# Kernel optimization log

Measured on AMD Instinct MI355X. Metric: run time of the kernel, lower is better.

Reference implementation:

```python
import jax, jax.numpy as jnp
import numpy as np

N = 6144
INPUT_SIZE = 1024
HIDDEN = 256
NEG_INF = -9e15  # matches torch masked_fill value -9000000000000000.0


def setup_inputs() -> dict:
    key = jax.random.key(0)
    k1, k2, k3, k4 = jax.random.split(key, 4)
    nodes_embed = jax.random.normal(k1, (N, INPUT_SIZE), dtype=jnp.float32)
    node_adj = jax.random.randint(k2, (N, N), 0, 2, dtype=jnp.int32)
    # learned params (xavier-uniform-ish scaling)
    limW = np.sqrt(6.0 / (INPUT_SIZE + HIDDEN))
    W = jax.random.uniform(k3, (INPUT_SIZE, HIDDEN), minval=-limW, maxval=limW, dtype=jnp.float32)
    lima = 1.414 * np.sqrt(6.0 / (2 * HIDDEN + 1))
    a_edge = jax.random.uniform(k4, (2 * HIDDEN,), minval=-lima, maxval=lima, dtype=jnp.float32)
    return {"nodes_embed": nodes_embed, "W": W, "a_edge": a_edge, "node_adj": node_adj}


def reference(nodes_embed, W, a_edge, node_adj):
    # h = nodes_embed @ W : [N, hidden]
    h = nodes_embed @ W
    # W_edge([h_i ; h_j]) decomposes exactly: (h_i @ a1) + (h_j @ a2)
    a1, a2 = a_edge[:HIDDEN], a_edge[HIDDEN:]
    score = (h @ a1)[:, None] + (h @ a2)[None, :]  # [N, N]
    adj_f = node_adj.astype(h.dtype)
    weight = jax.nn.leaky_relu(adj_f * score, negative_slope=0.2)
    weight = jnp.where(node_adj == 0, jnp.asarray(NEG_INF, h.dtype), weight)
    attention = jax.nn.softmax(weight, axis=-1)
    # dropout in eval mode (identity)
    return attention @ h  # [N, hidden]
```

## Files before the change

### kernel.cpp

```cpp
#include <hip/hip_runtime.h>
#include <hip/hip_bf16.h>

#define NN 6144
#define INPUT 1024
#define HID 256

using frag  = __attribute__((ext_vector_type(8))) short;
using f32x4 = __attribute__((ext_vector_type(4))) float;

static __device__ __forceinline__ unsigned short bf16u(float x) {
    unsigned u = __float_as_uint(x);
    u += 0x7fff + ((u >> 16) & 1);
    return (unsigned short)(u >> 16);
}

static __device__ __forceinline__ void gll16(const void* g, void* l) {
    __builtin_amdgcn_global_load_lds((__attribute__((address_space(1))) const void*)g,
                                     (__attribute__((address_space(3))) void*)l, 16, 0, 0);
}
static __device__ __forceinline__ void gll4(const void* g, void* l) {
    __builtin_amdgcn_global_load_lds((__attribute__((address_space(1))) const void*)g,
                                     (__attribute__((address_space(3))) void*)l, 4, 0, 0);
}

static __device__ __forceinline__ void lds_barrier() {
    asm volatile("s_waitcnt lgkmcnt(0)" ::: "memory");
    __builtin_amdgcn_s_barrier();
    __builtin_amdgcn_sched_barrier(0);
}

__global__ __launch_bounds__(256) void k_prep(const float* __restrict__ X,
                                              const float* __restrict__ W,
                                              unsigned short* __restrict__ Xb,
                                              unsigned short* __restrict__ Wt) {
    int b = blockIdx.x;
    if (b < 3072) {
        int t = b * 256 + threadIdx.x;
        const float4* p = reinterpret_cast<const float4*>(X) + (size_t)t * 2;
        float4 x0 = p[0], x1 = p[1];
        frag v;
        v[0] = (short)bf16u(x0.x); v[1] = (short)bf16u(x0.y);
        v[2] = (short)bf16u(x0.z); v[3] = (short)bf16u(x0.w);
        v[4] = (short)bf16u(x1.x); v[5] = (short)bf16u(x1.y);
        v[6] = (short)bf16u(x1.z); v[7] = (short)bf16u(x1.w);
        *reinterpret_cast<frag*>(Xb + (size_t)t * 8) = v;
    } else {
        int t = (b - 3072) * 256 + threadIdx.x;
        int n = t >> 10, k = t & 1023;
        Wt[t] = bf16u(W[k * HID + n]);
    }
}

__global__ __launch_bounds__(256, 4) void k_gemm1(const unsigned short* __restrict__ Xb,
                                                  const unsigned short* __restrict__ Wt,
                                                  const float* __restrict__ a_edge,
                                                  unsigned short* __restrict__ hT,
                                                  float* __restrict__ s1,
                                                  float* __restrict__ s2) {
    __shared__ unsigned short A[2][32][128];
    int t = threadIdx.x;
    int i0 = blockIdx.x * 32, n0 = blockIdx.y * 64;
    int w = t >> 6, l = t & 63, lm = l & 15, q = l >> 4;
    int nw = n0 + w * 16;

    const unsigned short* brow = Wt + (size_t)(nw + lm) * INPUT + q * 8;

    int r0 = w * 8 + (l >> 4);
    const unsigned short* xs0 = Xb + (size_t)(i0 + r0) * INPUT + (((l & 15) ^ (r0 & 7)) << 3);
    const unsigned short* xs1 = Xb + (size_t)(i0 + r0 + 4) * INPUT + (((l & 15) ^ ((r0 + 4) & 7)) << 3);

#define GSTAGE(C, BUF) { \
        gll16(xs0 + (C) * 128, &A[BUF][w * 8][0]); \
        gll16(xs1 + (C) * 128, &A[BUF][w * 8 + 4][0]); }

    f32x4 acc0 = {}, acc1 = {};
    GSTAGE(0, 0)

    for (int c = 0; c < 8; c++) {
        int buf = c & 1;
        frag b0 = *reinterpret_cast<const frag*>(brow + c * 128);
        frag b1 = *reinterpret_cast<const frag*>(brow + c * 128 + 32);
        frag b2 = *reinterpret_cast<const frag*>(brow + c * 128 + 64);
        frag b3 = *reinterpret_cast<const frag*>(brow + c * 128 + 96);
        asm volatile("s_waitcnt vmcnt(4)" ::: "memory");
        __builtin_amdgcn_s_barrier();
        __builtin_amdgcn_sched_barrier(0);
        if (c < 7) GSTAGE(c + 1, buf ^ 1)

#pragma unroll
        for (int kk = 0; kk < 4; kk++) {
            int sw = (kk * 32 + q * 8) ^ ((lm & 7) << 3);
            frag a0 = *reinterpret_cast<const frag*>(&A[buf][lm][sw]);
            frag a1 = *reinterpret_cast<const frag*>(&A[buf][16 + lm][sw]);
            frag b  = (kk == 0) ? b0 : (kk == 1) ? b1 : (kk == 2) ? b2 : b3;
            acc0 = __builtin_amdgcn_mfma_f32_16x16x32_bf16(a0, b, acc0, 0, 0, 0);
            acc1 = __builtin_amdgcn_mfma_f32_16x16x32_bf16(a1, b, acc1, 0, 0, 0);
        }
    }
#undef GSTAGE

    ushort4 o;
    o.x = bf16u(acc0[0]); o.y = bf16u(acc0[1]); o.z = bf16u(acc0[2]); o.w = bf16u(acc0[3]);
    *reinterpret_cast<ushort4*>(hT + (size_t)(nw + lm) * NN + i0 + q * 4) = o;
    o.x = bf16u(acc1[0]); o.y = bf16u(acc1[1]); o.z = bf16u(acc1[2]); o.w = bf16u(acc1[3]);
    *reinterpret_cast<ushort4*>(hT + (size_t)(nw + lm) * NN + i0 + 16 + q * 4) = o;

    float a1v = a_edge[nw + lm], a2v = a_edge[HID + nw + lm];
#pragma unroll
    for (int h = 0; h < 2; h++) {
        const f32x4& ac = h ? acc1 : acc0;
#pragma unroll
        for (int r = 0; r < 4; r++) {
            float v1 = ac[r] * a1v, v2 = ac[r] * a2v;
            v1 += __shfl_xor(v1, 1); v2 += __shfl_xor(v2, 1);
            v1 += __shfl_xor(v1, 2); v2 += __shfl_xor(v2, 2);
            v1 += __shfl_xor(v1, 4); v2 += __shfl_xor(v2, 4);
            v1 += __shfl_xor(v1, 8); v2 += __shfl_xor(v2, 8);
            if (lm == 0) {
                atomicAdd(&s1[i0 + h * 16 + q * 4 + r], v1);
                atomicAdd(&s2[i0 + h * 16 + q * 4 + r], v2);
            }
        }
    }
}

__global__ __launch_bounds__(512, 2) void k_attn(const int* __restrict__ adj,
                                                 const float* __restrict__ s1,
                                                 const float* __restrict__ s2,
                                                 const unsigned short* __restrict__ hT,
                                                 float* __restrict__ U4,
                                                 float* __restrict__ denom4) {
    __shared__ unsigned short P[2][32][136];
    __shared__ int   adjS[2][32][128];
    __shared__ float s2S[2][128];
    int t = threadIdx.x;
    int m = t >> 4, cg = t & 15;
    int i0 = blockIdx.x * 32;
    int q4 = blockIdx.y, j0 = q4 * 1536;
    int w = t >> 6, l = t & 63, lm = l & 15, q = l >> 4;

    float s1v = s1[i0 + m];
    const int*   astage = adj + (size_t)(i0 + w * 4 + (l >> 5)) * NN + j0 + (l & 31) * 4;
    const float* sstage = s2 + j0 + w * 16 + l;

    const unsigned short* brow[2];
#pragma unroll
    for (int nt = 0; nt < 2; nt++)
        brow[nt] = hT + (size_t)(w * 32 + nt * 16 + lm) * NN + j0 + q * 8;

    f32x4 acc[2][2] = {};
    float dsum = 0.f;

#define STAGE(JC, BUF) { \
        gll16(astage + (JC), &adjS[BUF][w * 4][0]); \
        gll16(astage + (JC) + 2 * NN, &adjS[BUF][w * 4 + 2][0]); \
        if (l < 16) gll4(sstage + (JC), &s2S[BUF][w * 16]); }

    STAGE(0, 0)

    for (int c = 0; c < 12; c++) {
        int buf = c & 1, jc = c * 128;

        frag bf[8];
#pragma unroll
        for (int kk = 0; kk < 4; kk++)
#pragma unroll
            for (int nt = 0; nt < 2; nt++)
                bf[kk * 2 + nt] = *reinterpret_cast<const frag*>(brow[nt] + jc + kk * 32);

        asm volatile("s_waitcnt vmcnt(8)" ::: "memory");
        __builtin_amdgcn_s_barrier();
        __builtin_amdgcn_sched_barrier(0);
        if (c < 11) STAGE(jc + 128, buf ^ 1)

        {
            const int*   aL = &adjS[buf][m][cg * 8];
            const float* sL = &s2S[buf][cg * 8];
            int4   av0 = *reinterpret_cast<const int4*>(aL);
            int4   av1 = *reinterpret_cast<const int4*>(aL + 4);
            float4 sv0 = *reinterpret_cast<const float4*>(sL);
            float4 sv1 = *reinterpret_cast<const float4*>(sL + 4);
            float sc, wv, p0, p1, p2, p3, p4, p5, p6, p7;
            sc = s1v + sv0.x; wv = fmaxf(sc, 0.2f * sc); p0 = av0.x ? __expf(wv) : 0.f;
            sc = s1v + sv0.y; wv = fmaxf(sc, 0.2f * sc); p1 = av0.y ? __expf(wv) : 0.f;
            sc = s1v + sv0.z; wv = fmaxf(sc, 0.2f * sc); p2 = av0.z ? __expf(wv) : 0.f;
            sc = s1v + sv0.w; wv = fmaxf(sc, 0.2f * sc); p3 = av0.w ? __expf(wv) : 0.f;
            sc = s1v + sv1.x; wv = fmaxf(sc, 0.2f * sc); p4 = av1.x ? __expf(wv) : 0.f;
            sc = s1v + sv1.y; wv = fmaxf(sc, 0.2f * sc); p5 = av1.y ? __expf(wv) : 0.f;
            sc = s1v + sv1.z; wv = fmaxf(sc, 0.2f * sc); p6 = av1.z ? __expf(wv) : 0.f;
            sc = s1v + sv1.w; wv = fmaxf(sc, 0.2f * sc); p7 = av1.w ? __expf(wv) : 0.f;
            dsum += ((p0 + p1) + (p2 + p3)) + ((p4 + p5) + (p6 + p7));
            frag pk;
            pk[0] = (short)bf16u(p0); pk[1] = (short)bf16u(p1);
            pk[2] = (short)bf16u(p2); pk[3] = (short)bf16u(p3);
            pk[4] = (short)bf16u(p4); pk[5] = (short)bf16u(p5);
            pk[6] = (short)bf16u(p6); pk[7] = (short)bf16u(p7);
            *reinterpret_cast<frag*>(&P[buf][m][cg * 8]) = pk;
        }

        lds_barrier();

        __builtin_amdgcn_s_setprio(1);
#pragma unroll
        for (int kk = 0; kk < 4; kk++) {
            frag a0 = *reinterpret_cast<const frag*>(&P[buf][lm][kk * 32 + q * 8]);
            frag a1 = *reinterpret_cast<const frag*>(&P[buf][16 + lm][kk * 32 + q * 8]);
#pragma unroll
            for (int nt = 0; nt < 2; nt++) {
                acc[0][nt] = __builtin_amdgcn_mfma_f32_16x16x32_bf16(a0, bf[kk * 2 + nt], acc[0][nt], 0, 0, 0);
                acc[1][nt] = __builtin_amdgcn_mfma_f32_16x16x32_bf16(a1, bf[kk * 2 + nt], acc[1][nt], 0, 0, 0);
            }
        }
        __builtin_amdgcn_s_setprio(0);
    }
#undef STAGE

    float v = dsum;
    v += __shfl_xor(v, 1); v += __shfl_xor(v, 2);
    v += __shfl_xor(v, 4); v += __shfl_xor(v, 8);
    if (cg == 0) denom4[(size_t)q4 * NN + i0 + m] = v;

    float* Ub = U4 + (size_t)q4 * NN * HID;
#pragma unroll
    for (int h = 0; h < 2; h++)
#pragma unroll
        for (int nt = 0; nt < 2; nt++)
#pragma unroll
            for (int r = 0; r < 4; r++)
                Ub[(size_t)(i0 + h * 16 + q * 4 + r) * HID + w * 32 + nt * 16 + lm] = acc[h][nt][r];
}

__global__ __launch_bounds__(256) void k_norm(const float* __restrict__ U4,
                                              const float* __restrict__ denom4,
                                              float* __restrict__ out) {
    int i = blockIdx.x, t = threadIdx.x;
    size_t S = (size_t)NN * HID;
    size_t base = (size_t)i * HID + t;
    float u = U4[base] + U4[base + S] + U4[base + 2 * S] + U4[base + 3 * S];
    float d = denom4[i] + denom4[i + NN] + denom4[i + 2 * NN] + denom4[i + 3 * NN];
    out[base] = (d != 0.f) ? u / d : 0.f;
}

extern "C" void kernel_launch(void* const* d_in, const int* in_sizes, int n_in,
                              void* d_out, int out_size, void* d_ws, size_t ws_size,
                              hipStream_t stream) {
    const float* X      = (const float*)d_in[0];
    const float* W      = (const float*)d_in[1];
    const float* a_edge = (const float*)d_in[2];
    const int*   adj    = (const int*)d_in[3];
    float* out = (float*)d_out;

    float* U4     = (float*)d_ws;
    float* denom4 = U4 + (size_t)4 * NN * HID;
    float* s1     = denom4 + (size_t)4 * NN;
    float* s2     = s1 + NN;
    unsigned short* hT = (unsigned short*)(s2 + NN);
    unsigned short* Wt = hT + (size_t)HID * NN;
    unsigned short* Xb = (unsigned short*)U4;

    hipMemsetAsync(s1, 0, 2 * NN * sizeof(float), stream);
    k_prep<<<3072 + INPUT * HID / 256, 256, 0, stream>>>(X, W, Xb, Wt);
    k_gemm1<<<dim3(NN / 32, HID / 64), 256, 0, stream>>>(Xb, Wt, a_edge, hT, s1, s2);
    k_attn<<<dim3(NN / 32, 4), 512, 0, stream>>>(adj, s1, s2, hT, U4, denom4);
    k_norm<<<NN, 256, 0, stream>>>(U4, denom4, out);
}
```

Baseline: 307.2 us.

## Pre-pack X, W and h into MFMA fragment tiles and drop LDS staging

The prep kernel now writes X and W in bf16 packed 16x32 fragment tiles, so each lane's MFMA operand sits in one contiguous 16-byte chunk. gemm1 streams these fragments straight from global memory into registers with a three-deep register prefetch, replacing the LDS double buffer and its barriers. gemm1 also writes h in the same fragment-tiled layout, and the attention kernel's B-operand loads become fully coalesced 512-element tile reads. The goal is to cut LDS traffic, barriers and strided global reads. In exchange, the W transpose in prep uses strided scalar reads, and the prefetch depth is fixed.

```diff
diff --git a/kernel.cpp b/kernel.cpp
--- a/kernel.cpp
+++ b/kernel.cpp
@@ -29,83 +29,81 @@
     __builtin_amdgcn_sched_barrier(0);
 }
 
+
 __global__ __launch_bounds__(256) void k_prep(const float* __restrict__ X,
                                               const float* __restrict__ W,
-                                              unsigned short* __restrict__ Xb,
-                                              unsigned short* __restrict__ Wt) {
+                                              unsigned short* __restrict__ Xbp,
+                                              unsigned short* __restrict__ Wtp) {
     int b = blockIdx.x;
     if (b < 3072) {
         int t = b * 256 + threadIdx.x;
-        const float4* p = reinterpret_cast<const float4*>(X) + (size_t)t * 2;
+        int i = t >> 7, k8 = t & 127;
+        const float4* p = reinterpret_cast<const float4*>(X + (size_t)i * INPUT + k8 * 8);
         float4 x0 = p[0], x1 = p[1];
         frag v;
         v[0] = (short)bf16u(x0.x); v[1] = (short)bf16u(x0.y);
         v[2] = (short)bf16u(x0.z); v[3] = (short)bf16u(x0.w);
         v[4] = (short)bf16u(x1.x); v[5] = (short)bf16u(x1.y);
         v[6] = (short)bf16u(x1.z); v[7] = (short)bf16u(x1.w);
-        *reinterpret_cast<frag*>(Xb + (size_t)t * 8) = v;
+        size_t off = ((size_t)((i >> 4) * 32 + (k8 >> 2))) * 512 + (k8 & 3) * 128 + (i & 15) * 8;
+        *reinterpret_cast<frag*>(Xbp + off) = v;
     } else {
-        int t = (b - 3072) * 256 + threadIdx.x;
-        int n = t >> 10, k = t & 1023;
-        Wt[t] = bf16u(W[k * HID + n]);
-    }
-}
-
-__global__ __launch_bounds__(256, 4) void k_gemm1(const unsigned short* __restrict__ Xb,
-                                                  const unsigned short* __restrict__ Wt,
+        int u = (b - 3072) * 256 + threadIdx.x;
+        int n = u >> 7, k8 = u & 127;
+        int k = k8 * 8;
+        frag v;
+#pragma unroll
+        for (int e = 0; e < 8; e++) v[e] = (short)bf16u(W[(size_t)(k + e) * HID + n]);
+        size_t off = ((size_t)((n >> 4) * 32 + (k8 >> 2))) * 512 + (k8 & 3) * 128 + (n & 15) * 8;
+        *reinterpret_cast<frag*>(Wtp + off) = v;
+    }
+}
+
+__global__ __launch_bounds__(256, 4) void k_gemm1(const unsigned short* __restrict__ Xbp,
+                                                  const unsigned short* __restrict__ Wtp,
                                                   const float* __restrict__ a_edge,
-                                                  unsigned short* __restrict__ hT,
+                                                  unsigned short* __restrict__ hTp,
                                                   float* __restrict__ s1,
                                                   float* __restrict__ s2) {
-    __shared__ unsigned short A[2][32][128];
     int t = threadIdx.x;
-    int i0 = blockIdx.x * 32, n0 = blockIdx.y * 64;
     int w = t >> 6, l = t & 63, lm = l & 15, q = l >> 4;
-    int nw = n0 + w * 16;
-
-    const unsigned short* brow = Wt + (size_t)(nw + lm) * INPUT + q * 8;
-
-    int r0 = w * 8 + (l >> 4);
-    const unsigned short* xs0 = Xb + (size_t)(i0 + r0) * INPUT + (((l & 15) ^ (r0 & 7)) << 3);
-    const unsigned short* xs1 = Xb + (size_t)(i0 + r0 + 4) * INPUT + (((l & 15) ^ ((r0 + 4) & 7)) << 3);
-
-#define GSTAGE(C, BUF) { \
-        gll16(xs0 + (C) * 128, &A[BUF][w * 8][0]); \
-        gll16(xs1 + (C) * 128, &A[BUF][w * 8 + 4][0]); }
+    int bx = blockIdx.x, by = blockIdx.y;
+    int i0 = bx * 32;
+    int tn = by * 4 + w;
+
+    const unsigned short* pA0 = Xbp + (size_t)(bx * 2) * 32 * 512 + l * 8;
+    const unsigned short* pA1 = Xbp + (size_t)(bx * 2 + 1) * 32 * 512 + l * 8;
+    const unsigned short* pB  = Wtp + (size_t)tn * 32 * 512 + l * 8;
 
     f32x4 acc0 = {}, acc1 = {};
-    GSTAGE(0, 0)
-
-    for (int c = 0; c < 8; c++) {
-        int buf = c & 1;
-        frag b0 = *reinterpret_cast<const frag*>(brow + c * 128);
-        frag b1 = *reinterpret_cast<const frag*>(brow + c * 128 + 32);
-        frag b2 = *reinterpret_cast<const frag*>(brow + c * 128 + 64);
-        frag b3 = *reinterpret_cast<const frag*>(brow + c * 128 + 96);
-        asm volatile("s_waitcnt vmcnt(4)" ::: "memory");
-        __builtin_amdgcn_s_barrier();
-        __builtin_amdgcn_sched_barrier(0);
-        if (c < 7) GSTAGE(c + 1, buf ^ 1)
-
-#pragma unroll
-        for (int kk = 0; kk < 4; kk++) {
-            int sw = (kk * 32 + q * 8) ^ ((lm & 7) << 3);
-            frag a0 = *reinterpret_cast<const frag*>(&A[buf][lm][sw]);
-            frag a1 = *reinterpret_cast<const frag*>(&A[buf][16 + lm][sw]);
-            frag b  = (kk == 0) ? b0 : (kk == 1) ? b1 : (kk == 2) ? b2 : b3;
-            acc0 = __builtin_amdgcn_mfma_f32_16x16x32_bf16(a0, b, acc0, 0, 0, 0);
-            acc1 = __builtin_amdgcn_mfma_f32_16x16x32_bf16(a1, b, acc1, 0, 0, 0);
-        }
-    }
-#undef GSTAGE
-
+    frag a0s[3], a1s[3], bs[3];
+#pragma unroll
+    for (int s = 0; s < 2; s++) {
+        a0s[s] = *reinterpret_cast<const frag*>(pA0 + s * 512);
+        a1s[s] = *reinterpret_cast<const frag*>(pA1 + s * 512);
+        bs[s]  = *reinterpret_cast<const frag*>(pB  + s * 512);
+    }
+#pragma unroll
+    for (int tk = 0; tk < 32; tk++) {
+        int cur = tk % 3;
+        if (tk < 30) {
+            int nx = (tk + 2) % 3;
+            a0s[nx] = *reinterpret_cast<const frag*>(pA0 + (tk + 2) * 512);
+            a1s[nx] = *reinterpret_cast<const frag*>(pA1 + (tk + 2) * 512);
+            bs[nx]  = *reinterpret_cast<const frag*>(pB  + (tk + 2) * 512);
+        }
+        acc0 = __builtin_amdgcn_mfma_f32_16x16x32_bf16(a0s[cur], bs[cur], acc0, 0, 0, 0);
+        acc1 = __builtin_amdgcn_mfma_f32_16x16x32_bf16(a1s[cur], bs[cur], acc1, 0, 0, 0);
+    }
+
+    unsigned short* tb = hTp + ((size_t)bx * 16 + tn) * 512;
     ushort4 o;
     o.x = bf16u(acc0[0]); o.y = bf16u(acc0[1]); o.z = bf16u(acc0[2]); o.w = bf16u(acc0[3]);
-    *reinterpret_cast<ushort4*>(hT + (size_t)(nw + lm) * NN + i0 + q * 4) = o;
+    *reinterpret_cast<ushort4*>(tb + (q >> 1) * 128 + lm * 8 + (q & 1) * 4) = o;
     o.x = bf16u(acc1[0]); o.y = bf16u(acc1[1]); o.z = bf16u(acc1[2]); o.w = bf16u(acc1[3]);
-    *reinterpret_cast<ushort4*>(hT + (size_t)(nw + lm) * NN + i0 + 16 + q * 4) = o;
-
-    float a1v = a_edge[nw + lm], a2v = a_edge[HID + nw + lm];
+    *reinterpret_cast<ushort4*>(tb + (2 + (q >> 1)) * 128 + lm * 8 + (q & 1) * 4) = o;
+
+    float a1v = a_edge[tn * 16 + lm], a2v = a_edge[HID + tn * 16 + lm];
 #pragma unroll
     for (int h = 0; h < 2; h++) {
         const f32x4& ac = h ? acc1 : acc0;
@@ -127,7 +125,7 @@
 __global__ __launch_bounds__(512, 2) void k_attn(const int* __restrict__ adj,
                                                  const float* __restrict__ s1,
                                                  const float* __restrict__ s2,
-                                                 const unsigned short* __restrict__ hT,
+                                                 const unsigned short* __restrict__ hTp,
                                                  float* __restrict__ U4,
                                                  float* __restrict__ denom4) {
     __shared__ unsigned short P[2][32][136];
@@ -143,10 +141,8 @@
     const int*   astage = adj + (size_t)(i0 + w * 4 + (l >> 5)) * NN + j0 + (l & 31) * 4;
     const float* sstage = s2 + j0 + w * 16 + l;
 
-    const unsigned short* brow[2];
-#pragma unroll
-    for (int nt = 0; nt < 2; nt++)
-        brow[nt] = hT + (size_t)(w * 32 + nt * 16 + lm) * NN + j0 + q * 8;
+    const unsigned short* hb = hTp + (size_t)(w * 2) * 512 + l * 8;
+    int tjb = q4 * 48;
 
     f32x4 acc[2][2] = {};
     float dsum = 0.f;
@@ -166,7 +162,8 @@
         for (int kk = 0; kk < 4; kk++)
 #pragma unroll
             for (int nt = 0; nt < 2; nt++)
-                bf[kk * 2 + nt] = *reinterpret_cast<const frag*>(brow[nt] + jc + kk * 32);
+                bf[kk * 2 + nt] = *reinterpret_cast<const frag*>(
+                    hb + ((size_t)(tjb + c * 4 + kk) * 16 + nt) * 512);
 
         asm volatile("s_waitcnt vmcnt(8)" ::: "memory");
         __builtin_amdgcn_s_barrier();
@@ -254,13 +251,13 @@
     float* denom4 = U4 + (size_t)4 * NN * HID;
     float* s1     = denom4 + (size_t)4 * NN;
     float* s2     = s1 + NN;
-    unsigned short* hT = (unsigned short*)(s2 + NN);
-    unsigned short* Wt = hT + (size_t)HID * NN;
-    unsigned short* Xb = (unsigned short*)U4;
+    unsigned short* hTp = (unsigned short*)(s2 + NN);
+    unsigned short* Wtp = hTp + (size_t)HID * NN;
+    unsigned short* Xbp = (unsigned short*)U4;
 
     hipMemsetAsync(s1, 0, 2 * NN * sizeof(float), stream);
-    k_prep<<<3072 + INPUT * HID / 256, 256, 0, stream>>>(X, W, Xb, Wt);
-    k_gemm1<<<dim3(NN / 32, HID / 64), 256, 0, stream>>>(Xb, Wt, a_edge, hT, s1, s2);
-    k_attn<<<dim3(NN / 32, 4), 512, 0, stream>>>(adj, s1, s2, hT, U4, denom4);
+    k_prep<<<3072 + 128, 256, 0, stream>>>(X, W, Xbp, Wtp);
+    k_gemm1<<<dim3(NN / 32, 4), 256, 0, stream>>>(Xbp, Wtp, a_edge, hTp, s1, s2);
+    k_attn<<<dim3(NN / 32, 4), 512, 0, stream>>>(adj, s1, s2, hTp, U4, denom4);
     k_norm<<<NN, 256, 0, stream>>>(U4, denom4, out);
 }
```

Measured after the change: 290.4 us. -5.5%, faster.
